# Kernel tuning notes

Measured on AMD Instinct MI355X. Metric: run time of the kernel, lower is better.

Reference implementation:

```python
import jax, jax.numpy as jnp
import numpy as np

_GROUP_SIZES = [4096, 2048, 1024, 8192, 512, 3072, 6144, 1024]
_K = 2048
_N = 2048


def setup_inputs() -> dict:
    key = jax.random.key(0)
    keys = jax.random.split(key, len(_GROUP_SIZES) + 1)
    inp = {}
    for i, m in enumerate(_GROUP_SIZES):
        inp[f"A{i}"] = jax.random.normal(keys[i], (m, _K), dtype=jnp.float32)
    inp["B_shared"] = jax.random.normal(keys[-1], (_K, _N), dtype=jnp.float32)
    return inp


def reference(A0, A1, A2, A3, A4, A5, A6, A7, B_shared):
    # torch: cat([a @ B for a in group_A], dim=0)
    # Concatenating ragged groups first and doing one GEMM is the same math
    # (row-block structure of matmul), expressed as a single fused contraction.
    A_cat = jnp.concatenate([A0, A1, A2, A3, A4, A5, A6, A7], axis=0)  # [M_total, K]
    return A_cat @ B_shared  # [M_total, N]
```

## Files before the change

kernel.cpp:

```cpp
#include <hip/hip_runtime.h>
#include <hip/hip_bf16.h>

using short8  = __attribute__((ext_vector_type(8))) short;
using ushort8 = __attribute__((ext_vector_type(8))) unsigned short;
using f32x4   = __attribute__((ext_vector_type(4))) float;

#define GLB(p)  ((const __attribute__((address_space(1))) void*)(p))
#define LDSP(p) ((__attribute__((address_space(3))) void*)(p))

static __device__ __forceinline__ unsigned short f2bf(float f) {
    union { float f; unsigned u; } v; v.f = f;
    unsigned u = v.u;
    u += 0x7fffu + ((u >> 16) & 1u);
    return (unsigned short)(u >> 16);
}

#define K_DIM 2048
#define N_DIM 2048
#define M_TOTAL 26112
#define N_GROUPS 8

__global__ __launch_bounds__(256) void cvt_a_kernel(const float* __restrict__ src,
                                                    unsigned short* __restrict__ dst) {
    long i = ((long)blockIdx.x * 256 + threadIdx.x) * 8;
    float4 x = *(const float4*)(src + i);
    float4 y = *(const float4*)(src + i + 4);
    ushort8 o;
    o[0] = f2bf(x.x); o[1] = f2bf(x.y); o[2] = f2bf(x.z); o[3] = f2bf(x.w);
    o[4] = f2bf(y.x); o[5] = f2bf(y.y); o[6] = f2bf(y.z); o[7] = f2bf(y.w);
    *(ushort8*)(dst + i) = o;
}

__global__ __launch_bounds__(256) void cvt_bt_kernel(const float* __restrict__ B,
                                                     unsigned short* __restrict__ Bt) {
    __shared__ float t[32][33];
    int bx = blockIdx.x, by = blockIdx.y;
    int tx = threadIdx.x, ty = threadIdx.y;
#pragma unroll
    for (int i = 0; i < 32; i += 8)
        t[ty + i][tx] = B[(long)(by * 32 + ty + i) * N_DIM + bx * 32 + tx];
    __syncthreads();
#pragma unroll
    for (int i = 0; i < 32; i += 8)
        Bt[(long)(bx * 32 + ty + i) * K_DIM + by * 32 + tx] = f2bf(t[tx][ty + i]);
}


#define PBAR() __builtin_amdgcn_s_barrier()
#define LGKM0() asm volatile("s_waitcnt lgkmcnt(0)" ::: "memory")
#define VMC(n)  asm volatile("s_waitcnt vmcnt(" #n ")" ::: "memory")

#define ST_A(BUF, H, L, TT)                                                        \
    __builtin_amdgcn_global_load_lds(                                              \
        GLB(aSt + (long)((H) * 128 + (L) * 64) * K_DIM + (TT) * 64),               \
        LDSP(lds + (BUF) * 32768 + (H) * 8192 + (L) * 4096 + w * 512), 16, 0, 0)
#define ST_B(BUF, H, L, TT)                                                        \
    __builtin_amdgcn_global_load_lds(                                              \
        GLB(bSt + (long)((H) * 128 + (L) * 64) * K_DIM + (TT) * 64),               \
        LDSP(lds + (BUF) * 32768 + 16384 + (H) * 8192 + (L) * 4096 + w * 512), 16, 0, 0)

#define TILE(BUF, T, DO1, DO2)                                                          \
    do {                                                                                \
        const unsigned short* pA = lds + (BUF) * 32768 + wm * 1024 + r16 * 64;          \
        const unsigned short* pB = lds + (BUF) * 32768 + 16384 + wn * 1024 + r16 * 64;  \
        short8 a0[4], a1[4], b00[2], b01[2], b10[2], b11[2];                            \
                      \
        _Pragma("unroll") for (int i = 0; i < 4; ++i) {                                 \
            a0[i] = *(const short8*)(pA + i * 2048 + c0 * 8);                           \
            a1[i] = *(const short8*)(pA + i * 2048 + c1 * 8);                           \
        }                                                                               \
        _Pragma("unroll") for (int j = 0; j < 2; ++j) {                                 \
            b00[j] = *(const short8*)(pB + j * 4096 + c0 * 8);                          \
            b01[j] = *(const short8*)(pB + j * 4096 + c1 * 8);                          \
        }                                                                               \
        if (DO1) { ST_A((BUF) ^ 1, 1, 0, (T) + 1); ST_A((BUF) ^ 1, 1, 1, (T) + 1); }    \
        PBAR(); LGKM0();                                                                \
        __builtin_amdgcn_s_setprio(1);                                                  \
        _Pragma("unroll") for (int j = 0; j < 2; ++j)                                   \
        _Pragma("unroll") for (int i = 0; i < 4; ++i) {                                 \
            acc[i][j] = __builtin_amdgcn_mfma_f32_16x16x32_bf16(a0[i], b00[j], acc[i][j], 0, 0, 0); \
            acc[i][j] = __builtin_amdgcn_mfma_f32_16x16x32_bf16(a1[i], b01[j], acc[i][j], 0, 0, 0); \
        }                                                                               \
        __builtin_amdgcn_s_setprio(0); PBAR();                                          \
                                    \
        _Pragma("unroll") for (int j = 0; j < 2; ++j) {                                 \
            b10[j] = *(const short8*)(pB + 8192 + j * 4096 + c0 * 8);                   \
            b11[j] = *(const short8*)(pB + 8192 + j * 4096 + c1 * 8);                   \
        }                                                                               \
        if (DO2) { ST_A((BUF), 0, 0, (T) + 2); ST_A((BUF), 0, 1, (T) + 2); }            \
        PBAR(); LGKM0();                                                                \
        __builtin_amdgcn_s_setprio(1);                                                  \
        _Pragma("unroll") for (int j = 0; j < 2; ++j)                                   \
        _Pragma("unroll") for (int i = 0; i < 4; ++i) {                                 \
            acc[i][j + 2] = __builtin_amdgcn_mfma_f32_16x16x32_bf16(a0[i], b10[j], acc[i][j + 2], 0, 0, 0); \
            acc[i][j + 2] = __builtin_amdgcn_mfma_f32_16x16x32_bf16(a1[i], b11[j], acc[i][j + 2], 0, 0, 0); \
        }                                                                               \
        __builtin_amdgcn_s_setprio(0); PBAR();                                          \
               \
        _Pragma("unroll") for (int i = 0; i < 4; ++i) {                                 \
            a0[i] = *(const short8*)(pA + 8192 + i * 2048 + c0 * 8);                    \
            a1[i] = *(const short8*)(pA + 8192 + i * 2048 + c1 * 8);                    \
        }                                                                               \
        if (DO2) { ST_B((BUF), 0, 0, (T) + 2); ST_B((BUF), 0, 1, (T) + 2); }            \
        PBAR(); LGKM0();                                                                \
        __builtin_amdgcn_s_setprio(1);                                                  \
        _Pragma("unroll") for (int j = 0; j < 2; ++j)                                   \
        _Pragma("unroll") for (int i = 0; i < 4; ++i) {                                 \
            acc[i + 4][j] = __builtin_amdgcn_mfma_f32_16x16x32_bf16(a0[i], b00[j], acc[i + 4][j], 0, 0, 0); \
            acc[i + 4][j] = __builtin_amdgcn_mfma_f32_16x16x32_bf16(a1[i], b01[j], acc[i + 4][j], 0, 0, 0); \
        }                                                                               \
        __builtin_amdgcn_s_setprio(0); PBAR();                                          \
                             \
        if (DO2) { ST_B((BUF), 1, 0, (T) + 2); ST_B((BUF), 1, 1, (T) + 2); }            \
        PBAR();                                                                         \
        __builtin_amdgcn_s_setprio(1);                                                  \
        _Pragma("unroll") for (int j = 0; j < 2; ++j)                                   \
        _Pragma("unroll") for (int i = 0; i < 4; ++i) {                                 \
            acc[i + 4][j + 2] = __builtin_amdgcn_mfma_f32_16x16x32_bf16(a0[i], b10[j], acc[i + 4][j + 2], 0, 0, 0); \
            acc[i + 4][j + 2] = __builtin_amdgcn_mfma_f32_16x16x32_bf16(a1[i], b11[j], acc[i + 4][j + 2], 0, 0, 0); \
        }                                                                               \
        __builtin_amdgcn_s_setprio(0);                                                  \
    } while (0)

__global__ __launch_bounds__(512, 2) void gemm8_kernel(const unsigned short* __restrict__ Acat,
                                                       const unsigned short* __restrict__ Bt,
                                                       float* __restrict__ C) {
    __shared__ unsigned short lds[65536];

    int wg  = blockIdx.x;
    int swz = (wg & 7) * 102 + (wg >> 3);
    int mt  = swz >> 3, nt = swz & 7;
    int m0  = mt * 256, n0 = nt * 256;

    int tid = threadIdx.x;
    int l   = tid & 63;
    int w   = tid >> 6;
    int wm  = w >> 2;
    int wn  = w & 3;
    int r16 = l & 15, kc = l >> 4, x = l & 7;
    int c0  = kc ^ x;
    int c1  = (4 + kc) ^ x;

    int srow = tid >> 3;
    int sq   = (tid & 7) ^ (srow & 7);
    const unsigned short* aSt = Acat + (long)(m0 + srow) * K_DIM + sq * 8;
    const unsigned short* bSt = Bt   + (long)(n0 + srow) * K_DIM + sq * 8;

    f32x4 acc[8][4] = {};

    ST_A(0, 0, 0, 0); ST_A(0, 0, 1, 0); ST_A(0, 1, 0, 0); ST_A(0, 1, 1, 0);
    ST_B(0, 0, 0, 0); ST_B(0, 0, 1, 0); ST_B(0, 1, 0, 0); ST_B(0, 1, 1, 0);
    ST_A(1, 0, 0, 1); ST_A(1, 0, 1, 1);
    ST_B(1, 0, 0, 1); ST_B(1, 0, 1, 1); ST_B(1, 1, 0, 1); ST_B(1, 1, 1, 1);
    VMC(6); PBAR();

#pragma unroll 1
    for (int t = 0; t < 30; t += 2) {
        TILE(0, t, 1, 1);     VMC(6); PBAR();
        TILE(1, t + 1, 1, 1); VMC(6); PBAR();
    }
    TILE(0, 30, 1, 0); VMC(0); PBAR();
    TILE(1, 31, 0, 0);

    int orow = m0 + wm * 16 + (l >> 4) * 4;
    int ocol = n0 + wn * 16 + (l & 15);
#pragma unroll
    for (int i = 0; i < 8; ++i)
#pragma unroll
        for (int j = 0; j < 4; ++j)
#pragma unroll
            for (int q = 0; q < 4; ++q)
                C[(long)(orow + i * 32 + q) * N_DIM + (ocol + j * 64)] = acc[i][j][q];
}

__global__ void naive_gemm_kernel(const float* __restrict__ A, const float* __restrict__ B,
                                  float* __restrict__ C, int M) {
    __shared__ float As[16][16];
    __shared__ float Bs[16][17];
    int tx = threadIdx.x, ty = threadIdx.y;
    int row = blockIdx.y * 16 + ty;
    int col = blockIdx.x * 16 + tx;
    float s = 0.f;
    for (int k0 = 0; k0 < K_DIM; k0 += 16) {
        As[ty][tx] = A[(long)row * K_DIM + k0 + tx];
        Bs[ty][tx] = B[(long)(k0 + ty) * N_DIM + col];
        __syncthreads();
#pragma unroll
        for (int t = 0; t < 16; ++t) s += As[ty][t] * Bs[t][tx];
        __syncthreads();
    }
    C[(long)row * N_DIM + col] = s;
}

extern "C" void kernel_launch(void* const* d_in, const int* in_sizes, int n_in,
                              void* d_out, int out_size, void* d_ws, size_t ws_size,
                              hipStream_t stream) {
    static const int g_m[N_GROUPS]   = {4096, 2048, 1024, 8192, 512, 3072, 6144, 1024};
    static const int g_off[N_GROUPS] = {0, 4096, 6144, 7168, 15360, 15872, 18944, 25088};

    float* C = (float*)d_out;
    const size_t need = ((size_t)M_TOTAL * K_DIM + (size_t)N_DIM * K_DIM) * 2;

    if (ws_size >= need) {
        unsigned short* Acat = (unsigned short*)d_ws;
        unsigned short* Bt   = Acat + (size_t)M_TOTAL * K_DIM;

        for (int g = 0; g < N_GROUPS; ++g)
            cvt_a_kernel<<<g_m[g], 256, 0, stream>>>((const float*)d_in[g],
                                                     Acat + (size_t)g_off[g] * K_DIM);
        cvt_bt_kernel<<<dim3(N_DIM / 32, K_DIM / 32), dim3(32, 8), 0, stream>>>(
            (const float*)d_in[8], Bt);

        gemm8_kernel<<<(M_TOTAL / 256) * (N_DIM / 256), 512, 0, stream>>>(Acat, Bt, C);
    } else {
        for (int g = 0; g < N_GROUPS; ++g)
            naive_gemm_kernel<<<dim3(N_DIM / 16, g_m[g] / 16), dim3(16, 16), 0, stream>>>(
                (const float*)d_in[g], (const float*)d_in[8], C + (size_t)g_off[g] * N_DIM,
                g_m[g]);
    }
}
```

Measured before the change: 307.3 us.

## Fuse fp32-to-bf16 A conversion into GEMM mainloop via register staging

Removes the eight separate A conversion kernels and the bf16 A workspace. The GEMM now reads fp32 A tiles straight from each group's input through registers, converts them to bf16 and writes them into the swizzled LDS buffer for the next k-tile. B still uses direct global-to-LDS loads, and the vmcnt waits are reworked around the register-staged A path. This saves a full write and re-read of a bf16 copy of A and several launches, in exchange for doubled A read bytes inside the GEMM, extra VGPR pressure and conversion ALU work in the mainloop.

```diff
diff --git a/kernel.cpp b/kernel.cpp
--- a/kernel.cpp
+++ b/kernel.cpp
@@ -14,22 +14,14 @@
     u += 0x7fffu + ((u >> 16) & 1u);
     return (unsigned short)(u >> 16);
 }
+static __device__ __forceinline__ unsigned short f2bfc(float f) {
+    return __builtin_bit_cast(unsigned short, __float2bfloat16(f));
+}
 
 #define K_DIM 2048
 #define N_DIM 2048
 #define M_TOTAL 26112
 #define N_GROUPS 8
-
-__global__ __launch_bounds__(256) void cvt_a_kernel(const float* __restrict__ src,
-                                                    unsigned short* __restrict__ dst) {
-    long i = ((long)blockIdx.x * 256 + threadIdx.x) * 8;
-    float4 x = *(const float4*)(src + i);
-    float4 y = *(const float4*)(src + i + 4);
-    ushort8 o;
-    o[0] = f2bf(x.x); o[1] = f2bf(x.y); o[2] = f2bf(x.z); o[3] = f2bf(x.w);
-    o[4] = f2bf(y.x); o[5] = f2bf(y.y); o[6] = f2bf(y.z); o[7] = f2bf(y.w);
-    *(ushort8*)(dst + i) = o;
-}
 
 __global__ __launch_bounds__(256) void cvt_bt_kernel(const float* __restrict__ B,
                                                      unsigned short* __restrict__ Bt) {
@@ -50,21 +42,45 @@
 #define LGKM0() asm volatile("s_waitcnt lgkmcnt(0)" ::: "memory")
 #define VMC(n)  asm volatile("s_waitcnt vmcnt(" #n ")" ::: "memory")
 
-#define ST_A(BUF, H, L, TT)                                                        \
-    __builtin_amdgcn_global_load_lds(                                              \
-        GLB(aSt + (long)((H) * 128 + (L) * 64) * K_DIM + (TT) * 64),               \
-        LDSP(lds + (BUF) * 32768 + (H) * 8192 + (L) * 4096 + w * 512), 16, 0, 0)
 #define ST_B(BUF, H, L, TT)                                                        \
     __builtin_amdgcn_global_load_lds(                                              \
         GLB(bSt + (long)((H) * 128 + (L) * 64) * K_DIM + (TT) * 64),               \
         LDSP(lds + (BUF) * 32768 + 16384 + (H) * 8192 + (L) * 4096 + w * 512), 16, 0, 0)
 
-#define TILE(BUF, T, DO1, DO2)                                                          \
+#define MMQ(MH, NH, AV, BV)                                                        \
+    _Pragma("unroll") for (int i = 0; i < 4; ++i)                                  \
+    _Pragma("unroll") for (int j = 0; j < 2; ++j)                                  \
+        acc[(MH) * 4 + i][(NH) * 2 + j] = __builtin_amdgcn_mfma_f32_16x16x32_bf16( \
+            AV[i], BV[j], acc[(MH) * 4 + i][(NH) * 2 + j], 0, 0, 0);
+
+#define ALOAD(T1)                                                                  \
+    do { const float* _ap = aLd + (T1) * 64;                                       \
+        ax0 = *(const float4*)(_ap);      ax1 = *(const float4*)(_ap + 4);         \
+        ax2 = *(const float4*)(_ap + 8);  ax3 = *(const float4*)(_ap + 12);        \
+        ax4 = *(const float4*)(_ap + 16); ax5 = *(const float4*)(_ap + 20);        \
+        ax6 = *(const float4*)(_ap + 24); ax7 = *(const float4*)(_ap + 28); } while (0)
+
+#define AWRITE(BWR)                                                                \
+    do { unsigned short* wb = lds + (BWR) * 32768 + awOfs;                         \
+        ushort8 o0, o1, o2, o3;                                                    \
+        o0[0]=f2bfc(ax0.x); o0[1]=f2bfc(ax0.y); o0[2]=f2bfc(ax0.z); o0[3]=f2bfc(ax0.w); \
+        o0[4]=f2bfc(ax1.x); o0[5]=f2bfc(ax1.y); o0[6]=f2bfc(ax1.z); o0[7]=f2bfc(ax1.w); \
+        o1[0]=f2bfc(ax2.x); o1[1]=f2bfc(ax2.y); o1[2]=f2bfc(ax2.z); o1[3]=f2bfc(ax2.w); \
+        o1[4]=f2bfc(ax3.x); o1[5]=f2bfc(ax3.y); o1[6]=f2bfc(ax3.z); o1[7]=f2bfc(ax3.w); \
+        o2[0]=f2bfc(ax4.x); o2[1]=f2bfc(ax4.y); o2[2]=f2bfc(ax4.z); o2[3]=f2bfc(ax4.w); \
+        o2[4]=f2bfc(ax5.x); o2[5]=f2bfc(ax5.y); o2[6]=f2bfc(ax5.z); o2[7]=f2bfc(ax5.w); \
+        o3[0]=f2bfc(ax6.x); o3[1]=f2bfc(ax6.y); o3[2]=f2bfc(ax6.z); o3[3]=f2bfc(ax6.w); \
+        o3[4]=f2bfc(ax7.x); o3[5]=f2bfc(ax7.y); o3[6]=f2bfc(ax7.z); o3[7]=f2bfc(ax7.w); \
+        *(ushort8*)(wb + wq0) = o0; *(ushort8*)(wb + wq1) = o1;                    \
+        *(ushort8*)(wb + wq2) = o2; *(ushort8*)(wb + wq3) = o3; } while (0)
+
+#define TILE(BUF, T, DOA, DOB)                                                          \
     do {                                                                                \
         const unsigned short* pA = lds + (BUF) * 32768 + wm * 1024 + r16 * 64;          \
         const unsigned short* pB = lds + (BUF) * 32768 + 16384 + wn * 1024 + r16 * 64;  \
         short8 a0[4], a1[4], b00[2], b01[2], b10[2], b11[2];                            \
-                      \
+        float4 ax0, ax1, ax2, ax3, ax4, ax5, ax6, ax7;                                  \
+                    \
         _Pragma("unroll") for (int i = 0; i < 4; ++i) {                                 \
             a0[i] = *(const short8*)(pA + i * 2048 + c0 * 8);                           \
             a1[i] = *(const short8*)(pA + i * 2048 + c1 * 8);                           \
@@ -73,64 +89,59 @@
             b00[j] = *(const short8*)(pB + j * 4096 + c0 * 8);                          \
             b01[j] = *(const short8*)(pB + j * 4096 + c1 * 8);                          \
         }                                                                               \
-        if (DO1) { ST_A((BUF) ^ 1, 1, 0, (T) + 1); ST_A((BUF) ^ 1, 1, 1, (T) + 1); }    \
+        if (DOA) ALOAD((T) + 1);                                                        \
         PBAR(); LGKM0();                                                                \
-        __builtin_amdgcn_s_setprio(1);                                                  \
-        _Pragma("unroll") for (int j = 0; j < 2; ++j)                                   \
-        _Pragma("unroll") for (int i = 0; i < 4; ++i) {                                 \
-            acc[i][j] = __builtin_amdgcn_mfma_f32_16x16x32_bf16(a0[i], b00[j], acc[i][j], 0, 0, 0); \
-            acc[i][j] = __builtin_amdgcn_mfma_f32_16x16x32_bf16(a1[i], b01[j], acc[i][j], 0, 0, 0); \
-        }                                                                               \
+        __builtin_amdgcn_s_setprio(1); MMQ(0, 0, a0, b00); MMQ(0, 0, a1, b01);          \
         __builtin_amdgcn_s_setprio(0); PBAR();                                          \
-                                    \
+                              \
         _Pragma("unroll") for (int j = 0; j < 2; ++j) {                                 \
             b10[j] = *(const short8*)(pB + 8192 + j * 4096 + c0 * 8);                   \
             b11[j] = *(const short8*)(pB + 8192 + j * 4096 + c1 * 8);                   \
         }                                                                               \
-        if (DO2) { ST_A((BUF), 0, 0, (T) + 2); ST_A((BUF), 0, 1, (T) + 2); }            \
+        if (DOB) { ST_B((BUF), 0, 0, (T) + 2); ST_B((BUF), 0, 1, (T) + 2); }            \
         PBAR(); LGKM0();                                                                \
-        __builtin_amdgcn_s_setprio(1);                                                  \
-        _Pragma("unroll") for (int j = 0; j < 2; ++j)                                   \
-        _Pragma("unroll") for (int i = 0; i < 4; ++i) {                                 \
-            acc[i][j + 2] = __builtin_amdgcn_mfma_f32_16x16x32_bf16(a0[i], b10[j], acc[i][j + 2], 0, 0, 0); \
-            acc[i][j + 2] = __builtin_amdgcn_mfma_f32_16x16x32_bf16(a1[i], b11[j], acc[i][j + 2], 0, 0, 0); \
-        }                                                                               \
+        __builtin_amdgcn_s_setprio(1); MMQ(0, 1, a0, b10); MMQ(0, 1, a1, b11);          \
         __builtin_amdgcn_s_setprio(0); PBAR();                                          \
-               \
+            \
         _Pragma("unroll") for (int i = 0; i < 4; ++i) {                                 \
             a0[i] = *(const short8*)(pA + 8192 + i * 2048 + c0 * 8);                    \
             a1[i] = *(const short8*)(pA + 8192 + i * 2048 + c1 * 8);                    \
         }                                                                               \
-        if (DO2) { ST_B((BUF), 0, 0, (T) + 2); ST_B((BUF), 0, 1, (T) + 2); }            \
+        if (DOB) { ST_B((BUF), 1, 0, (T) + 2); ST_B((BUF), 1, 1, (T) + 2); }            \
+        if (DOA) {                                                                      \
+            if (DOB) { VMC(4); } else { VMC(0); }                                       \
+            AWRITE((BUF) ^ 1);                                                          \
+        }                                                                               \
         PBAR(); LGKM0();                                                                \
-        __builtin_amdgcn_s_setprio(1);                                                  \
-        _Pragma("unroll") for (int j = 0; j < 2; ++j)                                   \
-        _Pragma("unroll") for (int i = 0; i < 4; ++i) {                                 \
-            acc[i + 4][j] = __builtin_amdgcn_mfma_f32_16x16x32_bf16(a0[i], b00[j], acc[i + 4][j], 0, 0, 0); \
-            acc[i + 4][j] = __builtin_amdgcn_mfma_f32_16x16x32_bf16(a1[i], b01[j], acc[i + 4][j], 0, 0, 0); \
-        }                                                                               \
+        __builtin_amdgcn_s_setprio(1); MMQ(1, 0, a0, b00); MMQ(1, 0, a1, b01);          \
         __builtin_amdgcn_s_setprio(0); PBAR();                                          \
-                             \
-        if (DO2) { ST_B((BUF), 1, 0, (T) + 2); ST_B((BUF), 1, 1, (T) + 2); }            \
-        PBAR();                                                                         \
-        __builtin_amdgcn_s_setprio(1);                                                  \
-        _Pragma("unroll") for (int j = 0; j < 2; ++j)                                   \
-        _Pragma("unroll") for (int i = 0; i < 4; ++i) {                                 \
-            acc[i + 4][j + 2] = __builtin_amdgcn_mfma_f32_16x16x32_bf16(a0[i], b10[j], acc[i + 4][j + 2], 0, 0, 0); \
-            acc[i + 4][j + 2] = __builtin_amdgcn_mfma_f32_16x16x32_bf16(a1[i], b11[j], acc[i + 4][j + 2], 0, 0, 0); \
-        }                                                                               \
+                                           \
+        __builtin_amdgcn_s_setprio(1); MMQ(1, 1, a0, b10); MMQ(1, 1, a1, b11);          \
         __builtin_amdgcn_s_setprio(0);                                                  \
     } while (0)
 
-__global__ __launch_bounds__(512, 2) void gemm8_kernel(const unsigned short* __restrict__ Acat,
-                                                       const unsigned short* __restrict__ Bt,
-                                                       float* __restrict__ C) {
+__global__ __launch_bounds__(512, 2) void gemm8_kernel(
+        const float* __restrict__ A0, const float* __restrict__ A1,
+        const float* __restrict__ A2, const float* __restrict__ A3,
+        const float* __restrict__ A4, const float* __restrict__ A5,
+        const float* __restrict__ A6, const float* __restrict__ A7,
+        const unsigned short* __restrict__ Bt, float* __restrict__ C) {
     __shared__ unsigned short lds[65536];
 
     int wg  = blockIdx.x;
     int swz = (wg & 7) * 102 + (wg >> 3);
     int mt  = swz >> 3, nt = swz & 7;
     int m0  = mt * 256, n0 = nt * 256;
+
+    const float* aBase; int goff;
+    if      (mt < 16) { aBase = A0; goff = 0;     }
+    else if (mt < 24) { aBase = A1; goff = 4096;  }
+    else if (mt < 28) { aBase = A2; goff = 6144;  }
+    else if (mt < 60) { aBase = A3; goff = 7168;  }
+    else if (mt < 62) { aBase = A4; goff = 15360; }
+    else if (mt < 74) { aBase = A5; goff = 15872; }
+    else if (mt < 98) { aBase = A6; goff = 18944; }
+    else              { aBase = A7; goff = 25088; }
 
     int tid = threadIdx.x;
     int l   = tid & 63;
@@ -143,23 +154,34 @@
 
     int srow = tid >> 3;
     int sq   = (tid & 7) ^ (srow & 7);
-    const unsigned short* aSt = Acat + (long)(m0 + srow) * K_DIM + sq * 8;
-    const unsigned short* bSt = Bt   + (long)(n0 + srow) * K_DIM + sq * 8;
+    const unsigned short* bSt = Bt + (long)(n0 + srow) * K_DIM + sq * 8;
+
+    const float* aLd = aBase + (long)(m0 - goff + (tid >> 1)) * K_DIM + (tid & 1) * 32;
+    int awOfs = (tid >> 1) * 64;
+    int wq0 = ((((tid & 1) * 4 + 0) ^ ((tid >> 1) & 7)) * 8);
+    int wq1 = ((((tid & 1) * 4 + 1) ^ ((tid >> 1) & 7)) * 8);
+    int wq2 = ((((tid & 1) * 4 + 2) ^ ((tid >> 1) & 7)) * 8);
+    int wq3 = ((((tid & 1) * 4 + 3) ^ ((tid >> 1) & 7)) * 8);
 
     f32x4 acc[8][4] = {};
 
-    ST_A(0, 0, 0, 0); ST_A(0, 0, 1, 0); ST_A(0, 1, 0, 0); ST_A(0, 1, 1, 0);
-    ST_B(0, 0, 0, 0); ST_B(0, 0, 1, 0); ST_B(0, 1, 0, 0); ST_B(0, 1, 1, 0);
-    ST_A(1, 0, 0, 1); ST_A(1, 0, 1, 1);
-    ST_B(1, 0, 0, 1); ST_B(1, 0, 1, 1); ST_B(1, 1, 0, 1); ST_B(1, 1, 1, 1);
-    VMC(6); PBAR();
+    {
+        float4 ax0, ax1, ax2, ax3, ax4, ax5, ax6, ax7;
+        ALOAD(0);
+        ST_B(0, 0, 0, 0); ST_B(0, 0, 1, 0); ST_B(0, 1, 0, 0); ST_B(0, 1, 1, 0);
+        ST_B(1, 0, 0, 1); ST_B(1, 0, 1, 1); ST_B(1, 1, 0, 1); ST_B(1, 1, 1, 1);
+        VMC(8);
+        AWRITE(0);
+        VMC(4);
+        LGKM0(); PBAR();
+    }
 
 #pragma unroll 1
     for (int t = 0; t < 30; t += 2) {
-        TILE(0, t, 1, 1);     VMC(6); PBAR();
-        TILE(1, t + 1, 1, 1); VMC(6); PBAR();
-    }
-    TILE(0, 30, 1, 0); VMC(0); PBAR();
+        TILE(0, t, 1, 1);     PBAR();
+        TILE(1, t + 1, 1, 1); PBAR();
+    }
+    TILE(0, 30, 1, 0); PBAR();
     TILE(1, 31, 0, 0);
 
     int orow = m0 + wm * 16 + (l >> 4) * 4;
@@ -199,19 +221,16 @@
     static const int g_off[N_GROUPS] = {0, 4096, 6144, 7168, 15360, 15872, 18944, 25088};
 
     float* C = (float*)d_out;
-    const size_t need = ((size_t)M_TOTAL * K_DIM + (size_t)N_DIM * K_DIM) * 2;
+    const size_t need = (size_t)N_DIM * K_DIM * 2;
 
     if (ws_size >= need) {
-        unsigned short* Acat = (unsigned short*)d_ws;
-        unsigned short* Bt   = Acat + (size_t)M_TOTAL * K_DIM;
-
-        for (int g = 0; g < N_GROUPS; ++g)
-            cvt_a_kernel<<<g_m[g], 256, 0, stream>>>((const float*)d_in[g],
-                                                     Acat + (size_t)g_off[g] * K_DIM);
+        unsigned short* Bt = (unsigned short*)d_ws;
         cvt_bt_kernel<<<dim3(N_DIM / 32, K_DIM / 32), dim3(32, 8), 0, stream>>>(
             (const float*)d_in[8], Bt);
-
-        gemm8_kernel<<<(M_TOTAL / 256) * (N_DIM / 256), 512, 0, stream>>>(Acat, Bt, C);
+        gemm8_kernel<<<(M_TOTAL / 256) * (N_DIM / 256), 512, 0, stream>>>(
+            (const float*)d_in[0], (const float*)d_in[1], (const float*)d_in[2],
+            (const float*)d_in[3], (const float*)d_in[4], (const float*)d_in[5],
+            (const float*)d_in[6], (const float*)d_in[7], Bt, C);
     } else {
         for (int g = 0; g < N_GROUPS; ++g)
             naive_gemm_kernel<<<dim3(N_DIM / 16, g_m[g] / 16), dim3(16, 16), 0, stream>>>(
```

Result: slower. 530.9 us (+72.7%).
